# Kernel optimization log

Hardware: AMD Instinct MI355X
Metric: run time of the kernel (lower is better)

## Reference

```python
import jax, jax.numpy as jnp
import numpy as np

NUM = 21  # classes 1..NUM scored; bin 0 is background, bin NUM+1 is a dump bin


def _class_counts(y_pred, y_true):
    # Single-pass histogram over all classes instead of O(num) full-tensor scans.
    yp = y_pred.ravel()
    yt = y_true.ravel()
    nbins = NUM + 2
    cnt_true = jnp.zeros((nbins,), jnp.float32).at[yt].add(1.0)
    cnt_pred = jnp.zeros((nbins,), jnp.float32).at[yp].add(1.0)
    # intersection: positions where pred == true, binned by label; mismatches -> dump bin
    inter_idx = jnp.where(yp == yt, yt, NUM + 1)
    inter = jnp.zeros((nbins,), jnp.float32).at[inter_idx].add(1.0)
    return cnt_true, cnt_pred, inter


def setup_inputs() -> dict:
    key = jax.random.key(0)
    k1, k2 = jax.random.split(key)
    shape = (32, 1024, 1024)
    y_pred = jax.random.randint(k1, shape, 0, NUM + 1, dtype=jnp.int32)
    y_true = jax.random.randint(k2, shape, 0, NUM + 1, dtype=jnp.int32)
    return {"y_pred": y_pred, "y_true": y_true}


def reference(y_pred, y_true):
    cnt_true, cnt_pred, inter = _class_counts(y_pred, y_true)
    # classes 1..NUM (label 0 skipped, as in the original loop over range(1, num+1))
    c_true = cnt_true[1:NUM + 1]
    c_pred = cnt_pred[1:NUM + 1]
    c_inter = inter[1:NUM + 1]
    union = c_true + c_pred - c_inter
    iou = (c_inter + 1e-6) / (union + 1e-6)  # [NUM]
    present = (c_true > 0).astype(jnp.float32)
    mIoU = jnp.sum(iou * present) / jnp.maximum(jnp.sum(present), 1.0)
    return mIoU, iou
```

## Files before the change

kernel.cpp:

```cpp
#include <hip/hip_runtime.h>


#define NUMC  21
#define NBINS 22
#define JBINS (NBINS * NBINS)
#define RSTR  485
#define NREP  4

__global__ void __launch_bounds__(256) hist_joint(
        const int* __restrict__ yp, const int* __restrict__ yt,
        unsigned int* __restrict__ partials, int n, int nblocks) {
    __shared__ unsigned int h[NREP * RSTR];
    for (int i = threadIdx.x; i < NREP * RSTR; i += 256) h[i] = 0u;
    __syncthreads();

    unsigned int* hh = h + (threadIdx.x >> 6) * RSTR;

    const int4* __restrict__ yp4 = (const int4*)yp;
    const int4* __restrict__ yt4 = (const int4*)yt;
    const int n4 = n >> 2;
    int tid = blockIdx.x * 256 + threadIdx.x;
    int stride = nblocks * 256;

    for (int i = tid; i < n4; i += stride) {
        int4 p = yp4[i];
        int4 t = yt4[i];
        atomicAdd(&hh[t.x * NBINS + p.x], 1u);
        atomicAdd(&hh[t.y * NBINS + p.y], 1u);
        atomicAdd(&hh[t.z * NBINS + p.z], 1u);
        atomicAdd(&hh[t.w * NBINS + p.w], 1u);
    }

    if (tid == 0) {
        for (int i = n4 << 2; i < n; i++)
            atomicAdd(&hh[yt[i] * NBINS + yp[i]], 1u);
    }

    __syncthreads();
    for (int c = threadIdx.x; c < JBINS; c += 256) {
        unsigned int s = 0;
        #pragma unroll
        for (int r = 0; r < NREP; r++) s += h[r * RSTR + c];
        partials[(size_t)blockIdx.x * JBINS + c] = s;
    }
}

__global__ void __launch_bounds__(256) reduce_partials(
        const unsigned int* __restrict__ partials,
        unsigned int* __restrict__ g, int nblocks) {
    __shared__ unsigned int lds[256];
    const int c = blockIdx.x;
    unsigned int s = 0;
    for (int b = threadIdx.x; b < nblocks; b += 256)
        s += partials[(size_t)b * JBINS + c];
    lds[threadIdx.x] = s;
    __syncthreads();
    for (int w = 128; w > 0; w >>= 1) {
        if (threadIdx.x < w) lds[threadIdx.x] += lds[threadIdx.x + w];
        __syncthreads();
    }
    if (threadIdx.x == 0) g[c] = lds[0];
}

__global__ void finalize_kernel(const unsigned int* __restrict__ g,
                                float* __restrict__ out) {
    int lane = threadIdx.x;
    float iou = 0.0f, pres = 0.0f;
    if (lane >= 1 && lane <= NUMC) {
        unsigned int ct = 0, cp = 0;
        #pragma unroll
        for (int k = 0; k < NBINS; k++) {
            ct += g[lane * NBINS + k];
            cp += g[k * NBINS + lane];
        }
        unsigned int ci = g[lane * NBINS + lane];
        float u = (float)ct + (float)cp - (float)ci;
        iou = ((float)ci + 1e-6f) / (u + 1e-6f);
        pres = (ct > 0u) ? 1.0f : 0.0f;
        out[lane] = iou;
    }
    float v = iou * pres, pc = pres;
    #pragma unroll
    for (int off = 32; off > 0; off >>= 1) {
        v += __shfl_down(v, off);
        pc += __shfl_down(pc, off);
    }
    if (lane == 0) out[0] = v / fmaxf(pc, 1.0f);
}

extern "C" void kernel_launch(void* const* d_in, const int* in_sizes, int n_in,
                              void* d_out, int out_size, void* d_ws, size_t ws_size,
                              hipStream_t stream) {
    const int* yp = (const int*)d_in[0];
    const int* yt = (const int*)d_in[1];
    int n = in_sizes[0];
    float* out = (float*)d_out;

    int nb = 2048;
    while (nb > 1 && (size_t)JBINS * 4 * ((size_t)nb + 1) > ws_size) nb >>= 1;
    unsigned int* g = (unsigned int*)d_ws;
    unsigned int* partials = g + JBINS;

    hist_joint<<<nb, 256, 0, stream>>>(yp, yt, partials, n, nb);
    reduce_partials<<<JBINS, 256, 0, stream>>>(partials, g, nb);
    finalize_kernel<<<1, 64, 0, stream>>>(g, out);
}
```

Measured before the change: 285.2 us.

## Replace partials reduction kernel with global atomics and unroll load loop

Drops the per-block partial histogram buffer and the separate reduction kernel. Each block now atomically adds its nonzero joint-histogram bins into a global array that is zeroed with an async memset. The main loop is also unrolled four ways so that eight vector loads are in flight before the shared-memory atomics. This trades one kernel launch and the partials traffic for contended global atomics, and it fixes the grid at 2048 blocks without checking the workspace size.

```diff
diff --git a/kernel.cpp b/kernel.cpp
--- a/kernel.cpp
+++ b/kernel.cpp
@@ -6,10 +6,11 @@
 #define JBINS (NBINS * NBINS)
 #define RSTR  485
 #define NREP  4
+#define GRID  2048
 
 __global__ void __launch_bounds__(256) hist_joint(
         const int* __restrict__ yp, const int* __restrict__ yt,
-        unsigned int* __restrict__ partials, int n, int nblocks) {
+        unsigned int* __restrict__ g, int n) {
     __shared__ unsigned int h[NREP * RSTR];
     for (int i = threadIdx.x; i < NREP * RSTR; i += 256) h[i] = 0u;
     __syncthreads();
@@ -19,47 +20,43 @@
     const int4* __restrict__ yp4 = (const int4*)yp;
     const int4* __restrict__ yt4 = (const int4*)yt;
     const int n4 = n >> 2;
-    int tid = blockIdx.x * 256 + threadIdx.x;
-    int stride = nblocks * 256;
+    const int stride = GRID * 256;
+    int i = blockIdx.x * 256 + threadIdx.x;
 
-    for (int i = tid; i < n4; i += stride) {
+#define DS4(P, T)                                  \
+    atomicAdd(&hh[(T).x * NBINS + (P).x], 1u);     \
+    atomicAdd(&hh[(T).y * NBINS + (P).y], 1u);     \
+    atomicAdd(&hh[(T).z * NBINS + (P).z], 1u);     \
+    atomicAdd(&hh[(T).w * NBINS + (P).w], 1u);
+
+    for (; i + 3 * stride < n4; i += 4 * stride) {
+        int4 p0 = yp4[i];
+        int4 p1 = yp4[i + stride];
+        int4 p2 = yp4[i + 2 * stride];
+        int4 p3 = yp4[i + 3 * stride];
+        int4 t0 = yt4[i];
+        int4 t1 = yt4[i + stride];
+        int4 t2 = yt4[i + 2 * stride];
+        int4 t3 = yt4[i + 3 * stride];
+        DS4(p0, t0) DS4(p1, t1) DS4(p2, t2) DS4(p3, t3)
+    }
+    for (; i < n4; i += stride) {
         int4 p = yp4[i];
         int4 t = yt4[i];
-        atomicAdd(&hh[t.x * NBINS + p.x], 1u);
-        atomicAdd(&hh[t.y * NBINS + p.y], 1u);
-        atomicAdd(&hh[t.z * NBINS + p.z], 1u);
-        atomicAdd(&hh[t.w * NBINS + p.w], 1u);
+        DS4(p, t)
     }
+#undef DS4
 
-    if (tid == 0) {
-        for (int i = n4 << 2; i < n; i++)
-            atomicAdd(&hh[yt[i] * NBINS + yp[i]], 1u);
+    if (blockIdx.x == 0 && threadIdx.x == 0) {
+        for (int k = n4 << 2; k < n; k++)
+            atomicAdd(&g[yt[k] * NBINS + yp[k]], 1u);
     }
 
     __syncthreads();
     for (int c = threadIdx.x; c < JBINS; c += 256) {
-        unsigned int s = 0;
-        #pragma unroll
-        for (int r = 0; r < NREP; r++) s += h[r * RSTR + c];
-        partials[(size_t)blockIdx.x * JBINS + c] = s;
+        unsigned int s = h[c] + h[RSTR + c] + h[2 * RSTR + c] + h[3 * RSTR + c];
+        if (s) atomicAdd(&g[c], s);
     }
-}
-
-__global__ void __launch_bounds__(256) reduce_partials(
-        const unsigned int* __restrict__ partials,
-        unsigned int* __restrict__ g, int nblocks) {
-    __shared__ unsigned int lds[256];
-    const int c = blockIdx.x;
-    unsigned int s = 0;
-    for (int b = threadIdx.x; b < nblocks; b += 256)
-        s += partials[(size_t)b * JBINS + c];
-    lds[threadIdx.x] = s;
-    __syncthreads();
-    for (int w = 128; w > 0; w >>= 1) {
-        if (threadIdx.x < w) lds[threadIdx.x] += lds[threadIdx.x + w];
-        __syncthreads();
-    }
-    if (threadIdx.x == 0) g[c] = lds[0];
 }
 
 __global__ void finalize_kernel(const unsigned int* __restrict__ g,
@@ -95,13 +92,9 @@
     const int* yt = (const int*)d_in[1];
     int n = in_sizes[0];
     float* out = (float*)d_out;
+    unsigned int* g = (unsigned int*)d_ws;
 
-    int nb = 2048;
-    while (nb > 1 && (size_t)JBINS * 4 * ((size_t)nb + 1) > ws_size) nb >>= 1;
-    unsigned int* g = (unsigned int*)d_ws;
-    unsigned int* partials = g + JBINS;
-
-    hist_joint<<<nb, 256, 0, stream>>>(yp, yt, partials, n, nb);
-    reduce_partials<<<JBINS, 256, 0, stream>>>(partials, g, nb);
+    hipMemsetAsync(g, 0, JBINS * sizeof(unsigned int), stream);
+    hist_joint<<<GRID, 256, 0, stream>>>(yp, yt, g, n);
     finalize_kernel<<<1, 64, 0, stream>>>(g, out);
 }
```

New measurement: 291.0 us. 1.02x slower.
